# Kernel optimization log

Measured on AMD Instinct MI355X. Metric: run time of the kernel, lower is better.

## Reference

```python
import jax, jax.numpy as jnp
import numpy as np

B, C, H, W = 4, 128, 64, 64
CO = 128

def setup_inputs() -> dict:
    key = jax.random.key(0)
    ks = jax.random.split(key, 10)
    s = 1.0 / np.sqrt(C)
    return {
        "x":  jax.random.normal(ks[0], (B, C, H, W), dtype=jnp.float32),
        "Wq": jax.random.uniform(ks[1], (C, C), jnp.float32, -s, s),
        "bq": jax.random.uniform(ks[2], (C,), jnp.float32, -s, s),
        "Wk": jax.random.uniform(ks[3], (C, C), jnp.float32, -s, s),
        "bk": jax.random.uniform(ks[4], (C,), jnp.float32, -s, s),
        "Wv": jax.random.uniform(ks[5], (C, C), jnp.float32, -s, s),
        "bv": jax.random.uniform(ks[6], (C,), jnp.float32, -s, s),
        "gamma": jnp.ones((1,), dtype=jnp.float32),
        "Wo": jax.random.uniform(ks[7], (CO, C), jnp.float32, -s, s),
        "bo": jax.random.uniform(ks[8], (CO,), jnp.float32, -s, s),
    }

def reference(x, Wq, bq, Wk, bk, Wv, bv, gamma, Wo, bo):
    b, c, h, w = x.shape
    xf = x.reshape(b, c, h * w)                       # [B,C,N]
    # 1x1 convs == channel matmuls
    Q = jnp.einsum('oc,bcn->bon', Wq, xf) + bq[None, :, None]
    K = jnp.einsum('oc,bcn->bon', Wk, xf) + bk[None, :, None]
    V = jnp.einsum('oc,bcn->bon', Wv, xf) + bv[None, :, None]
    # attention[b,i,j] = softmax_j( sum_c Q[b,c,i] K[b,c,j] )  (unscaled)
    scores = jnp.einsum('bci,bcj->bij', Q, K)         # [B,N,N]
    attn = jax.nn.softmax(scores, axis=-1)
    # selfAtten[b,c,i] = sum_j V[b,c,j] attn[b,i,j]
    sa = jnp.einsum('bcj,bij->bci', V, attn)          # [B,C,N]
    sa = gamma[0] * sa + xf
    out = jnp.einsum('oc,bcn->bon', Wo, sa) + bo[None, :, None]
    return out.reshape(b, Wo.shape[0], h, w)
```

## Files before the change

kernel.cpp:

```cpp
#include <hip/hip_runtime.h>

#define BB 4
#define CC 128
#define NN 4096

typedef float f32x4 __attribute__((ext_vector_type(4)));
typedef __bf16 bf16x8 __attribute__((ext_vector_type(8)));

#define MFMA16(A, B, C) __builtin_amdgcn_mfma_f32_16x16x32_bf16((A), (B), (C), 0, 0, 0)

typedef __attribute__((address_space(3))) void lds_void;
typedef __attribute__((address_space(1))) void glob_void;
#define GLD16(g, l) __builtin_amdgcn_global_load_lds((const glob_void*)(g), (lds_void*)(l), 16, 0, 0)

__device__ __forceinline__ int fK(int r) { return (r & 3) | (((r >> 3) & 1) << 2); }

__global__ __launch_bounds__(256)
void pack_w(const float* __restrict__ Wq, const float* __restrict__ bq,
            const float* __restrict__ Wk, const float* __restrict__ bk,
            const float* __restrict__ Wv, const float* __restrict__ bv,
            const float* __restrict__ Wo, const float* __restrict__ bo,
            __bf16* __restrict__ Wpk, float* __restrict__ bpk)
{
    const int mat = blockIdx.x >> 3;
    const int p   = blockIdx.x & 7;
    const int tid = threadIdx.x;
    const int ks  = tid >> 6;
    const int lane = tid & 63;
    const int col = lane & 15;
    const int quad = lane >> 4;

    const float LOG2E = 1.44269504088896340736f;
    const float* W = (mat == 0) ? Wq : (mat == 1) ? Wk : (mat == 2) ? Wv : Wo;
    const float* bsrc = (mat == 0) ? bq : (mat == 1) ? bk : (mat == 2) ? bv : bo;
    const float scale = (mat == 0) ? LOG2E : 1.0f;

    const float* wr = W + (size_t)(p * 16 + col) * CC + ks * 32 + quad * 8;
    float4 f0 = *(const float4*)wr;
    float4 f1 = *(const float4*)(wr + 4);
    bf16x8 a;
    a[0]=(__bf16)(f0.x*scale); a[1]=(__bf16)(f0.y*scale);
    a[2]=(__bf16)(f0.z*scale); a[3]=(__bf16)(f0.w*scale);
    a[4]=(__bf16)(f1.x*scale); a[5]=(__bf16)(f1.y*scale);
    a[6]=(__bf16)(f1.z*scale); a[7]=(__bf16)(f1.w*scale);
    *(bf16x8*)&Wpk[(((size_t)(mat * 8 + p) * 4 + ks) * 64 + lane) * 8] = a;

    if (p == 0 && tid < 128) bpk[mat * 128 + tid] = bsrc[tid] * scale;
}

__global__ __launch_bounds__(256, 2)
void qkv_gemm(const float* __restrict__ x,
              const __bf16* __restrict__ Wpk, const float* __restrict__ bpk,
              __bf16* __restrict__ Qt, __bf16* __restrict__ Kt,
              __bf16* __restrict__ Vblk)
{
    const int b    = blockIdx.y;
    const int n0   = blockIdx.x * 32;
    const int tid  = threadIdx.x;
    const int lane = tid & 63;
    const int wv   = __builtin_amdgcn_readfirstlane(tid >> 6);
    const int col  = lane & 15;
    const int quad = lane >> 4;

    __shared__ __bf16 xs[32 * 144];
    __shared__ __bf16 vs[128 * 32];

    {
        const int n  = tid & 31;
        const int c0 = tid >> 5;
        const float* xb = x + ((size_t)b * CC) * NN + n0 + n;
#pragma unroll
        for (int i = 0; i < 8; i++) {
            int c = (c0 + i * 8) * 2;
            float v0 = xb[(size_t)c * NN];
            float v1 = xb[(size_t)(c + 1) * NN];
            union { __bf16 h[2]; unsigned u; } pk;
            pk.h[0] = (__bf16)v0; pk.h[1] = (__bf16)v1;
            *(unsigned*)&xs[n * 144 + c] = pk.u;
        }
    }
    __syncthreads();

    bf16x8 Bf[2][4];
#pragma unroll
    for (int ng = 0; ng < 2; ng++)
#pragma unroll
        for (int ks = 0; ks < 4; ks++)
            Bf[ng][ks] = *(const bf16x8*)&xs[(ng * 16 + col) * 144 + ks * 32 + quad * 8];

#pragma unroll 1
    for (int p = 0; p < 6; p++) {
        const int mat = p >> 1;
        const int pg  = wv + 4 * (p & 1);
        const int o0  = pg * 16;

        bf16x8 Af[4];
#pragma unroll
        for (int ks = 0; ks < 4; ks++)
            Af[ks] = *(const bf16x8*)&Wpk[(((size_t)(mat * 8 + pg) * 4 + ks) * 64 + lane) * 8];

        f32x4 D[2];
#pragma unroll
        for (int ng = 0; ng < 2; ng++) D[ng] = (f32x4){0.f, 0.f, 0.f, 0.f};
#pragma unroll
        for (int ks = 0; ks < 4; ks++)
#pragma unroll
            for (int ng = 0; ng < 2; ng++)
                D[ng] = MFMA16(Af[ks], Bf[ng][ks], D[ng]);

        float4 bias = *(const float4*)(bpk + mat * 128 + o0 + quad * 4);

#pragma unroll
        for (int ng = 0; ng < 2; ng++) {
            const int n = ng * 16 + col;
            float v[4];
#pragma unroll
            for (int r = 0; r < 4; r++)
                v[r] = D[ng][r] + ((const float*)&bias)[r];
            if (mat == 0) {
                union { __bf16 h[4]; uint2 u; } pk;
                for (int r = 0; r < 4; r++) pk.h[r] = (__bf16)v[r];
                *(uint2*)&Qt[((size_t)b * NN + n0 + n) * CC + o0 + quad * 4] = pk.u;
            } else if (mat == 1) {
                const int rin = ((n0 & 32) + n) & 63;
                const int chunk = ((o0 + quad * 4) >> 3) ^ fK(rin);
                union { __bf16 h[4]; uint2 u; } pk;
                for (int r = 0; r < 4; r++) pk.h[r] = (__bf16)v[r];
                *(uint2*)&Kt[((size_t)b * NN + n0 + n) * CC + chunk * 8 + (quad & 1) * 4] = pk.u;
            } else {
#pragma unroll
                for (int r = 0; r < 4; r++)
                    vs[(o0 + quad * 4 + r) * 32 + n] = (__bf16)v[r];
            }
        }
    }
    __syncthreads();

    {
        __bf16* vd = Vblk + (((size_t)b * 64 + (n0 >> 6)) * CC) * 64;
        const int chbase = (n0 & 32) >> 3;
#pragma unroll
        for (int e = 0; e < 2; e++) {
            int idx = e * 256 + tid;
            int c = idx >> 2, chl = idx & 3;
            bf16x8 v = *(const bf16x8*)&vs[c * 32 + chl * 8];
            *(bf16x8*)&vd[c * 64 + (((chbase + chl) ^ (c & 7)) * 8)] = v;
        }
    }
}

__global__ __launch_bounds__(256, 3)
void flash_attn(const __bf16* __restrict__ Qt, const __bf16* __restrict__ Kt,
                const __bf16* __restrict__ Vblk,
                float* __restrict__ Opart, float* __restrict__ Lpart)
{
    const int blk = blockIdx.x;
    const int b    = blk & 3;
    const int jlow = (blk >> 2) & 1;
    const int jhigh = (blk >> 3) & 3;
    const int it32  = blk >> 5;
    const int js   = (jhigh << 1) | jlow;
    const int i0   = it32 * 128;

    const int tid  = threadIdx.x;
    const int lane = tid & 63;
    const int iw   = __builtin_amdgcn_readfirstlane(tid >> 6);
    const int col  = lane & 15;
    const int quad = lane >> 4;

    __shared__ __align__(16) char smem[34816];
    char* Kbytes = smem;
    char* Vbytes = smem + 16384;
    __bf16* Vh = (__bf16*)Vbytes;

#pragma unroll
    for (int e = 0; e < 4; e++) {
        int k = e * 256 + tid;
        Vh[128 * 64 + k] = (__bf16)((k < 64) ? 1.0f : 0.0f);
    }

    const __bf16* Qb = Qt + (size_t)b * NN * CC;
    const char*   Ks = (const char*)(Kt + (size_t)b * NN * CC);
    const char*   Vs = (const char*)(Vblk + ((size_t)b * 64 * CC) * 64);

    const int ibase = i0 + iw * 32;

    bf16x8 qf[2][4];
#pragma unroll
    for (int ig = 0; ig < 2; ig++)
#pragma unroll
        for (int ks = 0; ks < 4; ks++)
            qf[ig][ks] = *(const bf16x8*)(Qb + (size_t)(ibase + ig * 16 + col) * CC
                                             + ks * 32 + quad * 8);

    const int perm = ((col & 12) << 1) | (col & 3);
    const int fR   = fK(perm);
    int kaddr[4][4];
    const int joff[4] = {0, 4, 32, 36};
#pragma unroll
    for (int jg = 0; jg < 4; jg++)
#pragma unroll
        for (int ks = 0; ks < 4; ks++)
            kaddr[jg][ks] = (perm + joff[jg]) * 256 + (((ks * 4 + quad) ^ fR) * 16);
    int vaddr[8][2], oaddr[2];
#pragma unroll
    for (int cg = 0; cg < 8; cg++)
#pragma unroll
        for (int t = 0; t < 2; t++)
            vaddr[cg][t] = (cg * 16 + col) * 128 + (((t * 4 + quad) ^ (col & 7)) * 16);
#pragma unroll
    for (int t = 0; t < 2; t++)
        oaddr[t] = (128 + col) * 128 + (t * 4 + quad) * 16;

    f32x4 O[2][8], lacc[2];
#pragma unroll
    for (int ig = 0; ig < 2; ig++) {
#pragma unroll
        for (int cg = 0; cg < 8; cg++) O[ig][cg] = (f32x4){0.f, 0.f, 0.f, 0.f};
        lacc[ig] = (f32x4){0.f, 0.f, 0.f, 0.f};
    }

#pragma unroll 1
    for (int t8 = 0; t8 < 8; t8++) {
        const int jt = js * 8 + t8;
        const char* kg = Ks + (size_t)jt * 16384;
        const char* vg = Vs + (size_t)jt * 16384;
#pragma unroll
        for (int q = 0; q < 4; q++) {
            const int call = iw * 4 + q;
            GLD16(kg + call * 1024 + lane * 16, Kbytes + call * 1024 + lane * 16);
            GLD16(vg + call * 1024 + lane * 16, Vbytes + call * 1024 + lane * 16);
        }
        __syncthreads();

        f32x4 S[2][4];
#pragma unroll
        for (int ig = 0; ig < 2; ig++)
#pragma unroll
            for (int jg = 0; jg < 4; jg++)
                S[ig][jg] = (f32x4){-32.f, -32.f, -32.f, -32.f};
#pragma unroll
        for (int ks = 0; ks < 4; ks++) {
            bf16x8 k0 = *(const bf16x8*)(Kbytes + kaddr[0][ks]);
            bf16x8 k1 = *(const bf16x8*)(Kbytes + kaddr[1][ks]);
            bf16x8 k2 = *(const bf16x8*)(Kbytes + kaddr[2][ks]);
            bf16x8 k3 = *(const bf16x8*)(Kbytes + kaddr[3][ks]);
            S[0][0] = MFMA16(k0, qf[0][ks], S[0][0]);
            S[1][0] = MFMA16(k0, qf[1][ks], S[1][0]);
            S[0][1] = MFMA16(k1, qf[0][ks], S[0][1]);
            S[1][1] = MFMA16(k1, qf[1][ks], S[1][1]);
            S[0][2] = MFMA16(k2, qf[0][ks], S[0][2]);
            S[1][2] = MFMA16(k2, qf[1][ks], S[1][2]);
            S[0][3] = MFMA16(k3, qf[0][ks], S[0][3]);
            S[1][3] = MFMA16(k3, qf[1][ks], S[1][3]);
        }

#pragma unroll
        for (int ig = 0; ig < 2; ig++)
#pragma unroll
            for (int jg = 0; jg < 4; jg++)
#pragma unroll
                for (int r = 0; r < 4; r++)
                    S[ig][jg][r] = __builtin_amdgcn_exp2f(S[ig][jg][r]);

#pragma unroll
        for (int t = 0; t < 2; t++) {
            bf16x8 pf0, pf1;
#pragma unroll
            for (int e = 0; e < 8; e++) {
                int jg = 2 * t + (e >> 2), r = e & 3;
                pf0[e] = (__bf16)S[0][jg][r];
                pf1[e] = (__bf16)S[1][jg][r];
            }
#pragma unroll
            for (int cg = 0; cg < 8; cg++) {
                bf16x8 vf = *(const bf16x8*)(Vbytes + vaddr[cg][t]);
                O[0][cg] = MFMA16(vf, pf0, O[0][cg]);
                O[1][cg] = MFMA16(vf, pf1, O[1][cg]);
            }
            bf16x8 of = *(const bf16x8*)(Vbytes + oaddr[t]);
            lacc[0] = MFMA16(of, pf0, lacc[0]);
            lacc[1] = MFMA16(of, pf1, lacc[1]);
        }
        __syncthreads();
    }

    {
        float* Od = Opart + (((size_t)b * 8 + js) * CC) * NN + ibase;
#pragma unroll
        for (int ig = 0; ig < 2; ig++)
#pragma unroll
            for (int cg = 0; cg < 8; cg++)
#pragma unroll
                for (int r = 0; r < 4; r++)
                    Od[(size_t)(cg * 16 + quad * 4 + r) * NN + ig * 16 + col]
                        = O[ig][cg][r];
        if (quad == 0) {
            float* Ld = Lpart + ((size_t)b * 8 + js) * NN + ibase;
#pragma unroll
            for (int ig = 0; ig < 2; ig++)
                Ld[ig * 16 + col] = lacc[ig][0];
        }
    }
}

__global__ __launch_bounds__(256, 2)
void proj_out(const float* __restrict__ Opart, const float* __restrict__ Lpart,
              const float* __restrict__ x,
              const __bf16* __restrict__ Wpk, const float* __restrict__ bpk,
              const float* __restrict__ gamma, float* __restrict__ out)
{
    const int b    = blockIdx.y;
    const int n0   = blockIdx.x * 32;
    const int tid  = threadIdx.x;
    const int lane = tid & 63;
    const int wv   = __builtin_amdgcn_readfirstlane(tid >> 6);
    const int col  = lane & 15;
    const int quad = lane >> 4;

    __shared__ __bf16 sas[32 * 144];
    __shared__ float  outs[128 * 34];

    const float g = gamma[0];

    {
        const int n  = tid & 31;
        const int c0 = tid >> 5;
        const size_t nb = (size_t)b * 8;
        float l = 0.f;
#pragma unroll
        for (int jsp = 0; jsp < 8; jsp++)
            l += Lpart[(nb + jsp) * NN + n0 + n];
        const float gl = g / l;
        const float* xb = x + ((size_t)b * CC) * NN + n0 + n;
        const float* Ob = Opart + (nb * CC) * NN + n0 + n;
#pragma unroll
        for (int i = 0; i < 8; i++) {
            int c = (c0 + i * 8) * 2;
            float s0 = 0.f, s1 = 0.f;
#pragma unroll
            for (int jsp = 0; jsp < 8; jsp++) {
                s0 += Ob[((size_t)jsp * CC + c) * NN];
                s1 += Ob[((size_t)jsp * CC + c + 1) * NN];
            }
            float v0 = xb[(size_t)c * NN] + s0 * gl;
            float v1 = xb[(size_t)(c + 1) * NN] + s1 * gl;
            union { __bf16 h[2]; unsigned u; } pk;
            pk.h[0] = (__bf16)v0; pk.h[1] = (__bf16)v1;
            *(unsigned*)&sas[n * 144 + c] = pk.u;
        }
    }
    __syncthreads();

    bf16x8 Bf[2][4];
#pragma unroll
    for (int ng = 0; ng < 2; ng++)
#pragma unroll
        for (int ks = 0; ks < 4; ks++)
            Bf[ng][ks] = *(const bf16x8*)&sas[(ng * 16 + col) * 144 + ks * 32 + quad * 8];

#pragma unroll
    for (int p = 0; p < 2; p++) {
        const int pg = wv * 2 + p;
        const int o0 = pg * 16;
        bf16x8 Af[4];
#pragma unroll
        for (int ks = 0; ks < 4; ks++)
            Af[ks] = *(const bf16x8*)&Wpk[(((size_t)(3 * 8 + pg) * 4 + ks) * 64 + lane) * 8];

        f32x4 D[2];
#pragma unroll
        for (int ng = 0; ng < 2; ng++) D[ng] = (f32x4){0.f, 0.f, 0.f, 0.f};
#pragma unroll
        for (int ks = 0; ks < 4; ks++)
#pragma unroll
            for (int ng = 0; ng < 2; ng++)
                D[ng] = MFMA16(Af[ks], Bf[ng][ks], D[ng]);

        float4 bias = *(const float4*)(bpk + 3 * 128 + o0 + quad * 4);
#pragma unroll
        for (int ng = 0; ng < 2; ng++)
#pragma unroll
            for (int r = 0; r < 4; r++)
                outs[(o0 + quad * 4 + r) * 34 + ng * 16 + col]
                    = D[ng][r] + ((const float*)&bias)[r];
    }
    __syncthreads();

    {
        float* od = out + ((size_t)b * CC) * NN + n0;
#pragma unroll
        for (int e = 0; e < 16; e++) {
            int k = e * 256 + tid;
            int o = k >> 5, n = k & 31;
            od[(size_t)o * NN + n] = outs[o * 34 + n];
        }
    }
}

extern "C" void kernel_launch(void* const* d_in, const int* in_sizes, int n_in,
                              void* d_out, int out_size, void* d_ws, size_t ws_size,
                              hipStream_t stream)
{
    const float* x  = (const float*)d_in[0];
    const float* Wq = (const float*)d_in[1];
    const float* bq = (const float*)d_in[2];
    const float* Wk = (const float*)d_in[3];
    const float* bk = (const float*)d_in[4];
    const float* Wv = (const float*)d_in[5];
    const float* bv = (const float*)d_in[6];
    const float* gm = (const float*)d_in[7];
    const float* Wo = (const float*)d_in[8];
    const float* bo = (const float*)d_in[9];

    __bf16* Qt    = (__bf16*)d_ws;
    __bf16* Kt    = Qt + (size_t)BB * NN * CC;
    __bf16* Vblk  = Kt + (size_t)BB * NN * CC;
    float*  Opart = (float*)(Vblk + (size_t)BB * NN * CC);
    float*  Lpart = Opart + (size_t)32 * CC * NN;
    __bf16* Wpk   = (__bf16*)(Lpart + (size_t)32 * NN);
    float*  bpk   = (float*)(Wpk + 4 * 8 * 4 * 64 * 8);
    float*  out   = (float*)d_out;

    pack_w<<<32, 256, 0, stream>>>(Wq, bq, Wk, bk, Wv, bv, Wo, bo, Wpk, bpk);
    qkv_gemm<<<dim3(128, 4), 256, 0, stream>>>(x, Wpk, bpk, Qt, Kt, Vblk);
    flash_attn<<<1024, 256, 0, stream>>>(Qt, Kt, Vblk, Opart, Lpart);
    proj_out<<<dim3(128, 4), 256, 0, stream>>>(Opart, Lpart, x, Wpk, bpk, gm, out);
}
```

Measured before the change: 145.9 us.

## Store attention partials as bf16 via LDS staging, widen qkv_gemm to 512 threads

The flash-attention kernel now stages each block's O tile through LDS and writes it to global memory as bf16 in a tiled layout with coalesced 16-byte stores, instead of strided fp32 stores. proj_out reads that tiled bf16 layout. This halves the partial-output write and read traffic. qkv_gemm moves to 512 threads so that each wave handles one 16-row group per matrix instead of two, and flash_attn's occupancy hint rises from 3 to 4. Rounding the partial sums to bf16 before they are reduced costs some accuracy.

```diff
diff --git a/kernel.cpp b/kernel.cpp
--- a/kernel.cpp
+++ b/kernel.cpp
@@ -48,7 +48,7 @@
     if (p == 0 && tid < 128) bpk[mat * 128 + tid] = bsrc[tid] * scale;
 }
 
-__global__ __launch_bounds__(256, 2)
+__global__ __launch_bounds__(512, 2)
 void qkv_gemm(const float* __restrict__ x,
               const __bf16* __restrict__ Wpk, const float* __restrict__ bpk,
               __bf16* __restrict__ Qt, __bf16* __restrict__ Kt,
@@ -70,8 +70,8 @@
         const int c0 = tid >> 5;
         const float* xb = x + ((size_t)b * CC) * NN + n0 + n;
 #pragma unroll
-        for (int i = 0; i < 8; i++) {
-            int c = (c0 + i * 8) * 2;
+        for (int i = 0; i < 4; i++) {
+            int c = (c0 + i * 16) * 2;
             float v0 = xb[(size_t)c * NN];
             float v1 = xb[(size_t)(c + 1) * NN];
             union { __bf16 h[2]; unsigned u; } pk;
@@ -89,10 +89,9 @@
             Bf[ng][ks] = *(const bf16x8*)&xs[(ng * 16 + col) * 144 + ks * 32 + quad * 8];
 
 #pragma unroll 1
-    for (int p = 0; p < 6; p++) {
-        const int mat = p >> 1;
-        const int pg  = wv + 4 * (p & 1);
-        const int o0  = pg * 16;
+    for (int mat = 0; mat < 3; mat++) {
+        const int pg = wv;
+        const int o0 = pg * 16;
 
         bf16x8 Af[4];
 #pragma unroll
@@ -139,28 +138,25 @@
     {
         __bf16* vd = Vblk + (((size_t)b * 64 + (n0 >> 6)) * CC) * 64;
         const int chbase = (n0 & 32) >> 3;
-#pragma unroll
-        for (int e = 0; e < 2; e++) {
-            int idx = e * 256 + tid;
-            int c = idx >> 2, chl = idx & 3;
-            bf16x8 v = *(const bf16x8*)&vs[c * 32 + chl * 8];
-            *(bf16x8*)&vd[c * 64 + (((chbase + chl) ^ (c & 7)) * 8)] = v;
-        }
+        int idx = tid;
+        int c = idx >> 2, chl = idx & 3;
+        bf16x8 v = *(const bf16x8*)&vs[c * 32 + chl * 8];
+        *(bf16x8*)&vd[c * 64 + (((chbase + chl) ^ (c & 7)) * 8)] = v;
     }
 }
 
-__global__ __launch_bounds__(256, 3)
+__global__ __launch_bounds__(256, 4)
 void flash_attn(const __bf16* __restrict__ Qt, const __bf16* __restrict__ Kt,
                 const __bf16* __restrict__ Vblk,
-                float* __restrict__ Opart, float* __restrict__ Lpart)
+                __bf16* __restrict__ Opart, float* __restrict__ Lpart)
 {
     const int blk = blockIdx.x;
-    const int b    = blk & 3;
-    const int jlow = (blk >> 2) & 1;
-    const int jhigh = (blk >> 3) & 3;
-    const int it32  = blk >> 5;
-    const int js   = (jhigh << 1) | jlow;
-    const int i0   = it32 * 128;
+    const int b   = blk & 3;
+    const int jlo = (blk >> 2) & 1;
+    const int rr  = blk >> 3;
+    const int js  = ((rr & 3) << 1) | jlo;
+    const int it  = rr >> 2;
+    const int i0  = it * 128;
 
     const int tid  = threadIdx.x;
     const int lane = tid & 63;
@@ -176,7 +172,7 @@
 #pragma unroll
     for (int e = 0; e < 4; e++) {
         int k = e * 256 + tid;
-        Vh[128 * 64 + k] = (__bf16)((k < 64) ? 1.0f : 0.0f);
+        Vh[8192 + k] = (__bf16)((k < 64) ? 1.0f : 0.0f);
     }
 
     const __bf16* Qb = Qt + (size_t)b * NN * CC;
@@ -285,27 +281,33 @@
         __syncthreads();
     }
 
+    __bf16* Ol = (__bf16*)smem;
+#pragma unroll
+    for (int ig = 0; ig < 2; ig++) {
+#pragma unroll
+        for (int cg = 0; cg < 8; cg++)
+#pragma unroll
+            for (int r = 0; r < 4; r++)
+                Ol[(cg * 16 + quad * 4 + r) * 136 + iw * 32 + ig * 16 + col]
+                    = (__bf16)O[ig][cg][r];
+        if (quad == 0)
+            Lpart[((size_t)b * 8 + js) * NN + i0 + iw * 32 + ig * 16 + col]
+                = lacc[ig][0];
+    }
+    __syncthreads();
     {
-        float* Od = Opart + (((size_t)b * 8 + js) * CC) * NN + ibase;
-#pragma unroll
-        for (int ig = 0; ig < 2; ig++)
-#pragma unroll
-            for (int cg = 0; cg < 8; cg++)
-#pragma unroll
-                for (int r = 0; r < 4; r++)
-                    Od[(size_t)(cg * 16 + quad * 4 + r) * NN + ig * 16 + col]
-                        = O[ig][cg][r];
-        if (quad == 0) {
-            float* Ld = Lpart + ((size_t)b * 8 + js) * NN + ibase;
-#pragma unroll
-            for (int ig = 0; ig < 2; ig++)
-                Ld[ig * 16 + col] = lacc[ig][0];
+        __bf16* Od = Opart + (((size_t)(b * 8 + js) * 32 + it) * CC) * 128;
+#pragma unroll
+        for (int e = 0; e < 8; e++) {
+            int u = e * 256 + tid;
+            int c = u >> 4, ch = u & 15;
+            *(uint4*)&Od[c * 128 + ch * 8] = *(const uint4*)&Ol[c * 136 + ch * 8];
         }
     }
 }
 
 __global__ __launch_bounds__(256, 2)
-void proj_out(const float* __restrict__ Opart, const float* __restrict__ Lpart,
+void proj_out(const __bf16* __restrict__ Opart, const float* __restrict__ Lpart,
               const float* __restrict__ x,
               const __bf16* __restrict__ Wpk, const float* __restrict__ bpk,
               const float* __restrict__ gamma, float* __restrict__ out)
@@ -326,22 +328,24 @@
     {
         const int n  = tid & 31;
         const int c0 = tid >> 5;
-        const size_t nb = (size_t)b * 8;
+        const int it = n0 >> 7;
+        const int io = (n0 & 127) + n;
         float l = 0.f;
 #pragma unroll
         for (int jsp = 0; jsp < 8; jsp++)
-            l += Lpart[(nb + jsp) * NN + n0 + n];
+            l += Lpart[((size_t)b * 8 + jsp) * NN + n0 + n];
         const float gl = g / l;
         const float* xb = x + ((size_t)b * CC) * NN + n0 + n;
-        const float* Ob = Opart + (nb * CC) * NN + n0 + n;
+        const __bf16* Ob = Opart + (((size_t)(b * 8) * 32 + it) * CC) * 128;
 #pragma unroll
         for (int i = 0; i < 8; i++) {
             int c = (c0 + i * 8) * 2;
             float s0 = 0.f, s1 = 0.f;
 #pragma unroll
             for (int jsp = 0; jsp < 8; jsp++) {
-                s0 += Ob[((size_t)jsp * CC + c) * NN];
-                s1 += Ob[((size_t)jsp * CC + c + 1) * NN];
+                const __bf16* p = Ob + (size_t)jsp * (32 * CC * 128) + c * 128 + io;
+                s0 += (float)p[0];
+                s1 += (float)p[128];
             }
             float v0 = xb[(size_t)c * NN] + s0 * gl;
             float v1 = xb[(size_t)(c + 1) * NN] + s1 * gl;
@@ -416,14 +420,14 @@
     __bf16* Qt    = (__bf16*)d_ws;
     __bf16* Kt    = Qt + (size_t)BB * NN * CC;
     __bf16* Vblk  = Kt + (size_t)BB * NN * CC;
-    float*  Opart = (float*)(Vblk + (size_t)BB * NN * CC);
-    float*  Lpart = Opart + (size_t)32 * CC * NN;
+    __bf16* Opart = Vblk + (size_t)BB * NN * CC;
+    float*  Lpart = (float*)(Opart + (size_t)32 * 32 * CC * 128);
     __bf16* Wpk   = (__bf16*)(Lpart + (size_t)32 * NN);
     float*  bpk   = (float*)(Wpk + 4 * 8 * 4 * 64 * 8);
     float*  out   = (float*)d_out;
 
     pack_w<<<32, 256, 0, stream>>>(Wq, bq, Wk, bk, Wv, bv, Wo, bo, Wpk, bpk);
-    qkv_gemm<<<dim3(128, 4), 256, 0, stream>>>(x, Wpk, bpk, Qt, Kt, Vblk);
+    qkv_gemm<<<dim3(128, 4), 512, 0, stream>>>(x, Wpk, bpk, Qt, Kt, Vblk);
     flash_attn<<<1024, 256, 0, stream>>>(Qt, Kt, Vblk, Opart, Lpart);
     proj_out<<<dim3(128, 4), 256, 0, stream>>>(Opart, Lpart, x, Wpk, bpk, gm, out);
 }
```

After: 192.0 us. +31.6%, slower.
